# Kernel tuning notes

Measured on AMD Instinct MI355X. Metric: run time of the kernel, lower is better.

Reference implementation:

```python
import jax, jax.numpy as jnp
import numpy as np

SLEN, BSZ = 256, 8
NUM_HEAD, DIM_HEAD = 16, 64
IN_DIM = NUM_HEAD * DIM_HEAD  # 1024
LN_EPS = 1e-5


def setup_inputs() -> dict:
    key = jax.random.key(0)
    ks = jax.random.split(key, 6)
    std = 1.0 / np.sqrt(DIM_HEAD)
    std_q = 0.01 / np.sqrt(DIM_HEAD)
    beta_init = -1.0
    h = jax.random.normal(ks[0], (SLEN, BSZ, IN_DIM), dtype=jnp.float32)
    W_y = std * jax.random.normal(ks[1], (1, NUM_HEAD, DIM_HEAD, DIM_HEAD), dtype=jnp.float32)
    W_q = std_q * jax.random.normal(ks[2], (1, NUM_HEAD, DIM_HEAD, DIM_HEAD), dtype=jnp.float32)
    W_k = std * jax.random.normal(ks[3], (1, NUM_HEAD, DIM_HEAD, DIM_HEAD), dtype=jnp.float32)
    w_b = beta_init + std * jax.random.normal(ks[4], (1, NUM_HEAD, DIM_HEAD, 4), dtype=jnp.float32)
    out_w = std * jax.random.normal(ks[5], (IN_DIM, NUM_HEAD * DIM_HEAD), dtype=jnp.float32)
    ln_gamma = jnp.ones((IN_DIM,), dtype=jnp.float32)
    ln_beta = jnp.zeros((IN_DIM,), dtype=jnp.float32)
    return {"h": h, "W_y": W_y, "W_q": W_q, "W_k": W_k, "w_b": w_b,
            "out_w": out_w, "ln_gamma": ln_gamma, "ln_beta": ln_beta}


def _srwm_scan(x, W_y, W_q, W_k, w_b):
    # x: (slen, B, H, d); fast weights broadcast over batch
    bsz = x.shape[1]
    Wy0 = jnp.broadcast_to(W_y, (bsz,) + W_y.shape[1:])
    Wq0 = jnp.broadcast_to(W_q, (bsz,) + W_q.shape[1:])
    Wk0 = jnp.broadcast_to(W_k, (bsz,) + W_k.shape[1:])
    wb0 = jnp.broadcast_to(w_b, (bsz,) + w_b.shape[1:])

    def step(carry, x_t):
        Wy, Wq, Wk, wb = carry
        # generate outputs with W_{t-1}
        y = jnp.einsum('bhij,bhj->bhi', Wy, x_t)
        q = jax.nn.softmax(jnp.einsum('bhij,bhj->bhi', Wq, x_t), axis=-1)
        k = jax.nn.softmax(jnp.einsum('bhij,bhj->bhi', Wk, x_t), axis=-1)
        beta = jax.nn.sigmoid(jnp.einsum('bhjc,bhj->bhc', wb, x_t))  # (B,H,4)
        qmk = q - k
        def upd(W, b):
            dv = jnp.einsum('bhij,bhj->bhi', W, qmk)  # W q - W k
            return W + b[..., None, None] * dv[..., :, None] * k[..., None, :]
        Wy_n = upd(Wy, beta[..., 0])
        Wq_n = upd(Wq, beta[..., 1])
        Wk_n = upd(Wk, beta[..., 2])
        dvb = jnp.einsum('bhjc,bhj->bhc', wb, qmk)  # (B,H,4)
        wb_n = wb + beta[..., 3][..., None, None] * k[..., :, None] * dvb[..., None, :]
        return (Wy_n, Wq_n, Wk_n, wb_n), y

    _, ys = jax.lax.scan(step, (Wy0, Wq0, Wk0, wb0), x)
    return ys  # (slen, B, H, d)


def reference(h, W_y, W_q, W_k, w_b, out_w, ln_gamma, ln_beta):
    slen, bsz, _ = h.shape
    x = h.reshape(slen, bsz, NUM_HEAD, DIM_HEAD)
    ys = _srwm_scan(x, W_y, W_q, W_k, w_b)
    out = ys.reshape(slen, bsz, NUM_HEAD * DIM_HEAD)
    out = out @ out_w.T  # (slen, bsz, in_dim), no bias
    # dropout p=0 (eval): identity
    mu = jnp.mean(h, axis=-1, keepdims=True)
    var = jnp.mean(jnp.square(h - mu), axis=-1, keepdims=True)
    h_ln = (h - mu) * jax.lax.rsqrt(var + LN_EPS) * ln_gamma + ln_beta
    return h_ln + out
```

## Files before the change

### kernel.cpp

```cpp
#include <hip/hip_runtime.h>
#include <hip/hip_bf16.h>

#define SLEN  256
#define BSZ   8
#define NHEAD 16
#define DHEAD 64
#define INDIM 1024
#define LN_EPS 1e-5f

typedef __attribute__((ext_vector_type(4))) float f32x4;
typedef __attribute__((ext_vector_type(8))) short bf16x8;
typedef __attribute__((ext_vector_type(2))) float v2f;

__device__ __forceinline__ int f_as_i(float f) { union { float f; int i; } u; u.f = f; return u.i; }
__device__ __forceinline__ float i_as_f(int i) { union { float f; int i; } u; u.i = i; return u.f; }

__device__ __forceinline__ v2f fma2(v2f a, v2f b, v2f c) {
  return __builtin_elementwise_fma(a, b, c);
}

__device__ inline unsigned short f2bf(float x) {
  __hip_bfloat16 b = __float2bfloat16(x);
  union { __hip_bfloat16 b; unsigned short u; } cv;
  cv.b = b;
  return cv.u;
}

template <int CTRL>
__device__ __forceinline__ float dpp0(float x) {
  return i_as_f(__builtin_amdgcn_update_dpp(0, f_as_i(x), CTRL, 0xF, 0xF, true));
}
__device__ __forceinline__ float pair_other(float x) { return dpp0<0xB1>(x); }

__device__ __forceinline__ float wave_sum64(float v) {
  v += dpp0<0x111>(v);
  v += dpp0<0x112>(v);
  v += dpp0<0x114>(v);
  v += dpp0<0x118>(v);
  v += dpp0<0x142>(v);
  v += dpp0<0x143>(v);
  return i_as_f(__builtin_amdgcn_readlane(f_as_i(v), 63));
}

__global__ __launch_bounds__(512, 1) void scan_prep_k(
    const float* __restrict__ h,
    const float* __restrict__ Wy0,
    const float* __restrict__ Wq0,
    const float* __restrict__ Wk0,
    const float* __restrict__ wb0,
    const float* __restrict__ outw,
    const float* __restrict__ gamma,
    const float* __restrict__ lbeta,
    unsigned short* __restrict__ outw_bf,
    float* __restrict__ outp,
    unsigned short* __restrict__ ys_bf) {
  const int bid = blockIdx.x;
  const int tid = threadIdx.x;

  if (bid >= 128) {
    const int pb = bid - 128;
    if (pb < 512) {
      int i = (pb * 512 + tid) * 4;
      float4 v = *(const float4*)(outw + i);
      ushort4 o;
      o.x = f2bf(v.x); o.y = f2bf(v.y); o.z = f2bf(v.z); o.w = f2bf(v.w);
      *(ushort4*)(outw_bf + i) = o;
    } else {
      int r = pb - 512;
      const float* row = h + (size_t)r * INDIM;
      float2 v = *(const float2*)(row + tid * 2);
      float s  = v.x + v.y;
      float s2 = v.x * v.x + v.y * v.y;
      s  = wave_sum64(s);
      s2 = wave_sum64(s2);
      __shared__ float ls[8], ls2[8], sstat[2];
      int wvv = tid >> 6;
      if ((tid & 63) == 0) { ls[wvv] = s; ls2[wvv] = s2; }
      __syncthreads();
      if (tid == 0) {
        float S = 0.f, S2 = 0.f;
        #pragma unroll
        for (int i2 = 0; i2 < 8; ++i2) { S += ls[i2]; S2 += ls2[i2]; }
        float mu = S * (1.0f / INDIM);
        float var = S2 * (1.0f / INDIM) - mu * mu;
        sstat[0] = mu;
        sstat[1] = rsqrtf(var + LN_EPS);
      }
      __syncthreads();
      float mu = sstat[0], rs = sstat[1];
      float2 g2 = *(const float2*)(gamma + tid * 2);
      float2 b2 = *(const float2*)(lbeta + tid * 2);
      float2 o;
      o.x = (v.x - mu) * rs * g2.x + b2.x;
      o.y = (v.y - mu) * rs * g2.y + b2.y;
      *(float2*)(outp + (size_t)r * INDIM + tid * 2) = o;
    }
    return;
  }

  const int chain = bid;
  const int b    = chain >> 4;
  const int head = chain & 15;
  const int wv   = __builtin_amdgcn_readfirstlane(tid >> 6);
  const int lane = tid & 63;

  __shared__ __align__(16) float xbuf[3][64];
  __shared__ __align__(16) float eqk[2][2][64];
  __shared__ __align__(16) float meta[2][8];

  const float* xrow0 = h + (size_t)b * INDIM + head * DHEAD;

#define PUBLISH(T, V) {                                                          \
    if (m == 0) {                                                                \
      if (!(lane & 1))                                                           \
        ys_bf[(size_t)((T) * BSZ + b) * INDIM + head * DHEAD + r] = f2bf(V);     \
    } else {                                                                     \
      float e_ = __expf(V);                                                      \
      if (!(lane & 1)) eqk[(T) & 1][m - 1][r] = e_;                              \
      float sh_ = wave_sum64(e_) * 0.5f;                                         \
      if (lane == 0) meta[(T) & 1][(m - 1) * 2 + half] = sh_;                    \
    }                                                                            \
  }

#define PHASE(T, XC, XN) {                                                       \
    const int bp_ = ((T) - 1) & 1;                                               \
    float4 ss4 = *(const float4*)(&meta[bp_][0]);                                \
    float4 bb4 = *(const float4*)(&meta[bp_][4]);                                \
    v2f q2[16], k2[16];                                                          \
    _Pragma("unroll")                                                            \
    for (int g = 0; g < 8; ++g) {                                                \
      float4 qq = *(const float4*)(&eqk[bp_][0][j0 + g * 4]);                    \
      float4 kk = *(const float4*)(&eqk[bp_][1][j0 + g * 4]);                    \
      q2[2 * g] = (v2f){qq.x, qq.y}; q2[2 * g + 1] = (v2f){qq.z, qq.w};          \
      k2[2 * g] = (v2f){kk.x, kk.y}; k2[2 * g + 1] = (v2f){kk.z, kk.w};          \
    }                                                                            \
    if ((T) + 1 < SLEN) {                                                        \
      const float* xsrc_ = &xbuf[((T) + 1) % 3][j0];                             \
      _Pragma("unroll")                                                          \
      for (int g = 0; g < 8; ++g) {                                              \
        float4 x4_ = *(const float4*)(xsrc_ + g * 4);                            \
        XN[2 * g] = (v2f){x4_.x, x4_.y}; XN[2 * g + 1] = (v2f){x4_.z, x4_.w};    \
      }                                                                          \
    }                                                                            \
    v2f dqa = (v2f){0.f, 0.f}, dqb = (v2f){0.f, 0.f};                            \
    v2f dka = (v2f){0.f, 0.f}, dkb = (v2f){0.f, 0.f};                            \
    _Pragma("unroll")                                                            \
    for (int g = 0; g < 16; g += 2) {                                            \
      dqa = fma2(w2[g], q2[g], dqa);                                             \
      dqb = fma2(w2[g + 1], q2[g + 1], dqb);                                     \
      dka = fma2(w2[g], k2[g], dka);                                             \
      dkb = fma2(w2[g + 1], k2[g + 1], dkb);                                     \
    }                                                                            \
    float rq = __fdividef(1.f, ss4.x + ss4.y);                                   \
    float rk = __fdividef(1.f, ss4.z + ss4.w);                                   \
    v2f dqs = dqa + dqb, dks = dka + dkb;                                        \
    float dv = rq * (dqs.x + dqs.y) - rk * (dks.x + dks.y);                      \
    dv += pair_other(dv);                                                        \
    float bet_ = (m == 0) ? bb4.x : ((m == 1) ? bb4.y : bb4.z);                  \
    float c_ = bet_ * dv * rk;                                                   \
    v2f c2 = (v2f){c_, c_};                                                      \
    _Pragma("unroll")                                                            \
    for (int g = 0; g < 16; ++g) w2[g] = fma2(c2, k2[g], w2[g]);                 \
    v2f aa = (v2f){0.f, 0.f}, ab = (v2f){0.f, 0.f};                              \
    _Pragma("unroll")                                                            \
    for (int g = 0; g < 16; g += 2) {                                            \
      aa = fma2(w2[g], XC[g], aa);                                               \
      ab = fma2(w2[g + 1], XC[g + 1], ab);                                       \
    }                                                                            \
    v2f as = aa + ab;                                                            \
    float v_ = as.x + as.y;                                                      \
    v_ += pair_other(v_);                                                        \
    PUBLISH(T, v_);                                                              \
    __syncthreads();                                                             \
  }

  if (wv < 6) {
    const int m    = wv >> 1;
    const int half = wv & 1;
    const int r    = half * 32 + (lane >> 1);
    const int j0   = (lane & 1) * 32;
    const float* Wsel = (m == 0) ? Wy0 : ((m == 1) ? Wq0 : Wk0);
    const float* wrow = Wsel + (size_t)head * DHEAD * DHEAD + (size_t)r * DHEAD + j0;
    v2f w2[16];
    #pragma unroll
    for (int g = 0; g < 8; ++g) {
      float4 t4 = *(const float4*)(wrow + g * 4);
      w2[2 * g] = (v2f){t4.x, t4.y}; w2[2 * g + 1] = (v2f){t4.z, t4.w};
    }
    v2f xA[16], xB[16];
    #pragma unroll
    for (int g = 0; g < 8; ++g) {
      float4 t4 = *(const float4*)(xrow0 + j0 + g * 4);
      xA[2 * g] = (v2f){t4.x, t4.y}; xA[2 * g + 1] = (v2f){t4.z, t4.w};
    }
    __syncthreads();

    {
      v2f aa = (v2f){0.f, 0.f}, ab = (v2f){0.f, 0.f};
      #pragma unroll
      for (int g = 0; g < 16; g += 2) {
        aa = fma2(w2[g], xA[g], aa);
        ab = fma2(w2[g + 1], xA[g + 1], ab);
      }
      v2f as = aa + ab;
      float v0 = as.x + as.y;
      v0 += pair_other(v0);
      PUBLISH(0, v0);
      #pragma unroll
      for (int g = 0; g < 8; ++g) {
        float4 x4 = *(const float4*)(&xbuf[1][j0 + g * 4]);
        xB[2 * g] = (v2f){x4.x, x4.y}; xB[2 * g + 1] = (v2f){x4.z, x4.w};
      }
      __syncthreads();
    }
    for (int tt = 1; tt <= 253; tt += 2) {
      PHASE(tt, xB, xA);
      PHASE(tt + 1, xA, xB);
    }
    PHASE(255, xB, xA);
  } else if (wv == 6) {
    const float* wbrow = wb0 + (size_t)head * DHEAD * 4 + lane * 4;
    float4 wbv = *(const float4*)wbrow;
    const float* xl = h + (size_t)b * INDIM + head * DHEAD + lane;
    float xv = xl[0];
    float xn = xl[(size_t)BSZ * INDIM];
    float b3prev = 0.f;
    __syncthreads();

    {
      float p0 = wave_sum64(wbv.x * xv);
      float p1 = wave_sum64(wbv.y * xv);
      float p2 = wave_sum64(wbv.z * xv);
      float p3 = wave_sum64(wbv.w * xv);
      float b0 = __fdividef(1.f, 1.f + __expf(-p0));
      float b1 = __fdividef(1.f, 1.f + __expf(-p1));
      float b2 = __fdividef(1.f, 1.f + __expf(-p2));
      float b3 = __fdividef(1.f, 1.f + __expf(-p3));
      if (lane == 0) *(float4*)(&meta[0][4]) = (float4){b0, b1, b2, b3};
      b3prev = b3;
      xv = xn;
      xn = xl[(size_t)2 * BSZ * INDIM];
      __syncthreads();
    }
    for (int t = 1; t < SLEN; ++t) {
      const int bp = (t - 1) & 1;
      float4 ss4 = *(const float4*)(&meta[bp][0]);
      float eq = eqk[bp][0][lane];
      float ek = eqk[bp][1][lane];
      float rq = __fdividef(1.f, ss4.x + ss4.y);
      float rk = __fdividef(1.f, ss4.z + ss4.w);
      float qv = rq * eq, kv = rk * ek;
      float qmk = qv - kv;
      float g0 = wave_sum64(wbv.x * qmk);
      float g1 = wave_sum64(wbv.y * qmk);
      float g2 = wave_sum64(wbv.z * qmk);
      float g3 = wave_sum64(wbv.w * qmk);
      float cl = b3prev * kv;
      wbv.x += cl * g0; wbv.y += cl * g1; wbv.z += cl * g2; wbv.w += cl * g3;
      float p0 = wave_sum64(wbv.x * xv);
      float p1 = wave_sum64(wbv.y * xv);
      float p2 = wave_sum64(wbv.z * xv);
      float p3 = wave_sum64(wbv.w * xv);
      float b0 = __fdividef(1.f, 1.f + __expf(-p0));
      float b1 = __fdividef(1.f, 1.f + __expf(-p1));
      float b2 = __fdividef(1.f, 1.f + __expf(-p2));
      float b3 = __fdividef(1.f, 1.f + __expf(-p3));
      if (lane == 0) *(float4*)(&meta[t & 1][4]) = (float4){b0, b1, b2, b3};
      b3prev = b3;
      xv = xn;
      if (t + 2 < SLEN) xn = xl[(size_t)(t + 2) * BSZ * INDIM];
      __syncthreads();
    }
  } else {
    xbuf[1][lane] = xrow0[(size_t)BSZ * INDIM + lane];
    xbuf[2][lane] = xrow0[(size_t)2 * BSZ * INDIM + lane];
    float g1 = xrow0[(size_t)3 * BSZ * INDIM + lane];
    __syncthreads();

    for (int t = 0; t < SLEN; ++t) {
      if (t + 3 < SLEN) xbuf[t % 3][lane] = g1;
      if (t + 4 < SLEN) g1 = xrow0[(size_t)(t + 4) * BSZ * INDIM + lane];
      __syncthreads();
    }
  }
#undef PHASE
#undef PUBLISH
}

#define LDA 40
__global__ __launch_bounds__(256, 2) void gemm_acc_k(
    const unsigned short* __restrict__ A,
    const unsigned short* __restrict__ B,
    float* __restrict__ out,
    float scale) {
  __shared__ __align__(16) unsigned short Al[2][64 * LDA];
  __shared__ __align__(16) unsigned short Bl[2][64 * LDA];

  const int bid0 = blockIdx.x;
  const int swz = (bid0 & 7) * 64 + (bid0 >> 3);
  const int bx = swz & 15;
  const int by = swz >> 4;
  const int tid = threadIdx.x;
  const int wave = tid >> 6, lane = tid & 63;
  const int wr = wave >> 1, wc = wave & 1;
  const int l16 = lane & 15;
  const int kofs = (lane >> 4) * 8;

  const short* Ap = (const short*)A;
  const short* Bp = (const short*)B;

  const int srow = tid >> 2;
  const int scol = (tid & 3) * 8;
  const short* ags = Ap + (size_t)(by * 64 + srow) * INDIM + scol;
  const short* bgs = Bp + (size_t)(bx * 64 + srow) * INDIM + scol;
  unsigned short* adst = &Al[0][srow * LDA + scol];
  unsigned short* bdst = &Bl[0][srow * LDA + scol];

  f32x4 acc[2][2];
  #pragma unroll
  for (int i = 0; i < 2; ++i)
    #pragma unroll
    for (int j = 0; j < 2; ++j)
      acc[i][j] = (f32x4){0.f, 0.f, 0.f, 0.f};

  {
    uint4 ga = *(const uint4*)(ags);
    uint4 gb = *(const uint4*)(bgs);
    *(uint4*)(adst) = ga;
    *(uint4*)(bdst) = gb;
  }
  __syncthreads();

  int buf = 0;
  for (int it = 0; it < 32; ++it) {
    uint4 ga, gb;
    const bool more = (it + 1 < 32);
    if (more) {
      ga = *(const uint4*)(ags + (it + 1) * 32);
      gb = *(const uint4*)(bgs + (it + 1) * 32);
    }
    bf16x8 af[2], bfv[2];
    #pragma unroll
    for (int i = 0; i < 2; ++i)
      af[i] = *(const bf16x8*)(&Al[buf][(wr * 32 + i * 16 + l16) * LDA + kofs]);
    #pragma unroll
    for (int j = 0; j < 2; ++j)
      bfv[j] = *(const bf16x8*)(&Bl[buf][(wc * 32 + j * 16 + l16) * LDA + kofs]);
    #pragma unroll
    for (int i = 0; i < 2; ++i)
      #pragma unroll
      for (int j = 0; j < 2; ++j)
        acc[i][j] = __builtin_amdgcn_mfma_f32_16x16x32_bf16(af[i], bfv[j], acc[i][j], 0, 0, 0);
    if (more) {
      *(uint4*)(adst + (buf ^ 1) * 64 * LDA) = ga;
      *(uint4*)(bdst + (buf ^ 1) * 64 * LDA) = gb;
    }
    __syncthreads();
    buf ^= 1;
  }

  const int rq4 = (lane >> 4) * 4;
  #pragma unroll
  for (int i = 0; i < 2; ++i) {
    #pragma unroll
    for (int reg = 0; reg < 4; ++reg) {
      int r = by * 64 + wr * 32 + i * 16 + rq4 + reg;
      #pragma unroll
      for (int j = 0; j < 2; ++j) {
        int n = bx * 64 + wc * 32 + j * 16 + l16;
        size_t idx = (size_t)r * INDIM + n;
        out[idx] += acc[i][j][reg] * scale;
      }
    }
  }
}

extern "C" void kernel_launch(void* const* d_in, const int* in_sizes, int n_in,
                              void* d_out, int out_size, void* d_ws, size_t ws_size,
                              hipStream_t stream) {
  const float* h    = (const float*)d_in[0];
  const float* Wy   = (const float*)d_in[1];
  const float* Wq   = (const float*)d_in[2];
  const float* Wk   = (const float*)d_in[3];
  const float* wb   = (const float*)d_in[4];
  const float* outw = (const float*)d_in[5];
  const float* gam  = (const float*)d_in[6];
  const float* bet  = (const float*)d_in[7];
  float* out = (float*)d_out;

  char* ws = (char*)d_ws;
  unsigned short* ys_bf   = (unsigned short*)ws;
  unsigned short* outw_bf = (unsigned short*)(ws + (size_t)2048 * 1024 * 2);

  scan_prep_k<<<128 + 512 + 2048, 512, 0, stream>>>(h, Wy, Wq, Wk, wb, outw,
                                                    gam, bet, outw_bf, out, ys_bf);
  gemm_acc_k<<<512, 256, 0, stream>>>(ys_bf, outw_bf, out, 1e-38f);
  gemm_acc_k<<<512, 256, 0, stream>>>(ys_bf, outw_bf, out, 1.0f);
}
```

Measured before the change: 306.9 us.

## Shorten scan step dependency chain, widen GEMM K-tile, drop duplicate GEMM launch

The scan step now computes W·x and k·x from the old weights and forms y as A + c·(k·x). This takes the post-update matvec off the serial dependency chain after the weight update, and it switches to 4-wide vector FMAs. The GEMM now uses a 64-wide K tile per stage, giving half as many barrier iterations. The extra GEMM launch with a tiny scale factor is removed, so the GEMM runs once instead of twice. The algebraic rewrite changes floating-point rounding slightly, and the larger tile uses more LDS.

```diff
diff --git a/kernel.cpp b/kernel.cpp
--- a/kernel.cpp
+++ b/kernel.cpp
@@ -10,14 +10,14 @@
 
 typedef __attribute__((ext_vector_type(4))) float f32x4;
 typedef __attribute__((ext_vector_type(8))) short bf16x8;
-typedef __attribute__((ext_vector_type(2))) float v2f;
 
 __device__ __forceinline__ int f_as_i(float f) { union { float f; int i; } u; u.f = f; return u.i; }
 __device__ __forceinline__ float i_as_f(int i) { union { float f; int i; } u; u.i = i; return u.f; }
 
-__device__ __forceinline__ v2f fma2(v2f a, v2f b, v2f c) {
+__device__ __forceinline__ f32x4 fma4(f32x4 a, f32x4 b, f32x4 c) {
   return __builtin_elementwise_fma(a, b, c);
 }
+__device__ __forceinline__ float hsum4(f32x4 a) { return (a.x + a.y) + (a.z + a.w); }
 
 __device__ inline unsigned short f2bf(float x) {
   __hip_bfloat16 b = __float2bfloat16(x);
@@ -124,52 +124,46 @@
 
 #define PHASE(T, XC, XN) {                                                       \
     const int bp_ = ((T) - 1) & 1;                                               \
+    const f32x4* eq4_ = (const f32x4*)(&eqk[bp_][0][j0]);                        \
+    const f32x4* ek4_ = (const f32x4*)(&eqk[bp_][1][j0]);                        \
+    f32x4 q4[8], k4[8];                                                          \
+    _Pragma("unroll")                                                            \
+    for (int g = 0; g < 8; ++g) { q4[g] = eq4_[g]; k4[g] = ek4_[g]; }            \
     float4 ss4 = *(const float4*)(&meta[bp_][0]);                                \
     float4 bb4 = *(const float4*)(&meta[bp_][4]);                                \
-    v2f q2[16], k2[16];                                                          \
+    if ((T) + 1 < SLEN) {                                                        \
+      const f32x4* xs_ = (const f32x4*)(&xbuf[((T) + 1) % 3][j0]);               \
+      _Pragma("unroll")                                                          \
+      for (int g = 0; g < 8; ++g) XN[g] = xs_[g];                                \
+    }                                                                            \
+    f32x4 mva = (f32x4){0.f, 0.f, 0.f, 0.f};                                     \
+    f32x4 mvb = (f32x4){0.f, 0.f, 0.f, 0.f};                                     \
+    _Pragma("unroll")                                                            \
+    for (int g = 0; g < 8; g += 2) {                                             \
+      mva = fma4(w4[g], XC[g], mva);                                             \
+      mvb = fma4(w4[g + 1], XC[g + 1], mvb);                                     \
+    }                                                                            \
+    f32x4 dqa = (f32x4){0.f, 0.f, 0.f, 0.f};                                     \
+    f32x4 dka = (f32x4){0.f, 0.f, 0.f, 0.f};                                     \
+    f32x4 exa = (f32x4){0.f, 0.f, 0.f, 0.f};                                     \
     _Pragma("unroll")                                                            \
     for (int g = 0; g < 8; ++g) {                                                \
-      float4 qq = *(const float4*)(&eqk[bp_][0][j0 + g * 4]);                    \
-      float4 kk = *(const float4*)(&eqk[bp_][1][j0 + g * 4]);                    \
-      q2[2 * g] = (v2f){qq.x, qq.y}; q2[2 * g + 1] = (v2f){qq.z, qq.w};          \
-      k2[2 * g] = (v2f){kk.x, kk.y}; k2[2 * g + 1] = (v2f){kk.z, kk.w};          \
-    }                                                                            \
-    if ((T) + 1 < SLEN) {                                                        \
-      const float* xsrc_ = &xbuf[((T) + 1) % 3][j0];                             \
-      _Pragma("unroll")                                                          \
-      for (int g = 0; g < 8; ++g) {                                              \
-        float4 x4_ = *(const float4*)(xsrc_ + g * 4);                            \
-        XN[2 * g] = (v2f){x4_.x, x4_.y}; XN[2 * g + 1] = (v2f){x4_.z, x4_.w};    \
-      }                                                                          \
-    }                                                                            \
-    v2f dqa = (v2f){0.f, 0.f}, dqb = (v2f){0.f, 0.f};                            \
-    v2f dka = (v2f){0.f, 0.f}, dkb = (v2f){0.f, 0.f};                            \
-    _Pragma("unroll")                                                            \
-    for (int g = 0; g < 16; g += 2) {                                            \
-      dqa = fma2(w2[g], q2[g], dqa);                                             \
-      dqb = fma2(w2[g + 1], q2[g + 1], dqb);                                     \
-      dka = fma2(w2[g], k2[g], dka);                                             \
-      dkb = fma2(w2[g + 1], k2[g + 1], dkb);                                     \
+      dqa = fma4(w4[g], q4[g], dqa);                                             \
+      dka = fma4(w4[g], k4[g], dka);                                             \
+      exa = fma4(k4[g], XC[g], exa);                                             \
     }                                                                            \
     float rq = __fdividef(1.f, ss4.x + ss4.y);                                   \
     float rk = __fdividef(1.f, ss4.z + ss4.w);                                   \
-    v2f dqs = dqa + dqb, dks = dka + dkb;                                        \
-    float dv = rq * (dqs.x + dqs.y) - rk * (dks.x + dks.y);                      \
+    float dv = rq * hsum4(dqa) - rk * hsum4(dka);                                \
     dv += pair_other(dv);                                                        \
     float bet_ = (m == 0) ? bb4.x : ((m == 1) ? bb4.y : bb4.z);                  \
     float c_ = bet_ * dv * rk;                                                   \
-    v2f c2 = (v2f){c_, c_};                                                      \
+    f32x4 c4_ = (f32x4){c_, c_, c_, c_};                                         \
     _Pragma("unroll")                                                            \
-    for (int g = 0; g < 16; ++g) w2[g] = fma2(c2, k2[g], w2[g]);                 \
-    v2f aa = (v2f){0.f, 0.f}, ab = (v2f){0.f, 0.f};                              \
-    _Pragma("unroll")                                                            \
-    for (int g = 0; g < 16; g += 2) {                                            \
-      aa = fma2(w2[g], XC[g], aa);                                               \
-      ab = fma2(w2[g + 1], XC[g + 1], ab);                                       \
-    }                                                                            \
-    v2f as = aa + ab;                                                            \
-    float v_ = as.x + as.y;                                                      \
-    v_ += pair_other(v_);                                                        \
+    for (int g = 0; g < 8; ++g) w4[g] = fma4(c4_, k4[g], w4[g]);                 \
+    float A_ = hsum4(mva + mvb); A_ += pair_other(A_);                           \
+    float B_ = hsum4(exa);       B_ += pair_other(B_);                           \
+    float v_ = A_ + c_ * B_;                                                     \
     PUBLISH(T, v_);                                                              \
     __syncthreads();                                                             \
   }
@@ -181,36 +175,28 @@
     const int j0   = (lane & 1) * 32;
     const float* Wsel = (m == 0) ? Wy0 : ((m == 1) ? Wq0 : Wk0);
     const float* wrow = Wsel + (size_t)head * DHEAD * DHEAD + (size_t)r * DHEAD + j0;
-    v2f w2[16];
-    #pragma unroll
-    for (int g = 0; g < 8; ++g) {
-      float4 t4 = *(const float4*)(wrow + g * 4);
-      w2[2 * g] = (v2f){t4.x, t4.y}; w2[2 * g + 1] = (v2f){t4.z, t4.w};
-    }
-    v2f xA[16], xB[16];
-    #pragma unroll
-    for (int g = 0; g < 8; ++g) {
-      float4 t4 = *(const float4*)(xrow0 + j0 + g * 4);
-      xA[2 * g] = (v2f){t4.x, t4.y}; xA[2 * g + 1] = (v2f){t4.z, t4.w};
-    }
+    f32x4 w4[8];
+    #pragma unroll
+    for (int g = 0; g < 8; ++g) w4[g] = *(const f32x4*)(wrow + g * 4);
+    f32x4 xA[8], xB[8];
+    #pragma unroll
+    for (int g = 0; g < 8; ++g) xA[g] = *(const f32x4*)(xrow0 + j0 + g * 4);
     __syncthreads();
 
     {
-      v2f aa = (v2f){0.f, 0.f}, ab = (v2f){0.f, 0.f};
-      #pragma unroll
-      for (int g = 0; g < 16; g += 2) {
-        aa = fma2(w2[g], xA[g], aa);
-        ab = fma2(w2[g + 1], xA[g + 1], ab);
+      const f32x4* xs = (const f32x4*)(&xbuf[1][j0]);
+      #pragma unroll
+      for (int g = 0; g < 8; ++g) xB[g] = xs[g];
+      f32x4 aa = (f32x4){0.f, 0.f, 0.f, 0.f};
+      f32x4 ab = (f32x4){0.f, 0.f, 0.f, 0.f};
+      #pragma unroll
+      for (int g = 0; g < 8; g += 2) {
+        aa = fma4(w4[g], xA[g], aa);
+        ab = fma4(w4[g + 1], xA[g + 1], ab);
       }
-      v2f as = aa + ab;
-      float v0 = as.x + as.y;
+      float v0 = hsum4(aa + ab);
       v0 += pair_other(v0);
       PUBLISH(0, v0);
-      #pragma unroll
-      for (int g = 0; g < 8; ++g) {
-        float4 x4 = *(const float4*)(&xbuf[1][j0 + g * 4]);
-        xB[2 * g] = (v2f){x4.x, x4.y}; xB[2 * g + 1] = (v2f){x4.z, x4.w};
-      }
       __syncthreads();
     }
     for (int tt = 1; tt <= 253; tt += 2) {
@@ -287,14 +273,13 @@
 #undef PUBLISH
 }
 
-#define LDA 40
+#define GLDA 72
 __global__ __launch_bounds__(256, 2) void gemm_acc_k(
     const unsigned short* __restrict__ A,
     const unsigned short* __restrict__ B,
-    float* __restrict__ out,
-    float scale) {
-  __shared__ __align__(16) unsigned short Al[2][64 * LDA];
-  __shared__ __align__(16) unsigned short Bl[2][64 * LDA];
+    float* __restrict__ out) {
+  __shared__ __align__(16) unsigned short Al[2][64 * GLDA];
+  __shared__ __align__(16) unsigned short Bl[2][64 * GLDA];
 
   const int bid0 = blockIdx.x;
   const int swz = (bid0 & 7) * 64 + (bid0 >> 3);
@@ -310,11 +295,11 @@
   const short* Bp = (const short*)B;
 
   const int srow = tid >> 2;
-  const int scol = (tid & 3) * 8;
+  const int scol = (tid & 3) * 16;
   const short* ags = Ap + (size_t)(by * 64 + srow) * INDIM + scol;
   const short* bgs = Bp + (size_t)(bx * 64 + srow) * INDIM + scol;
-  unsigned short* adst = &Al[0][srow * LDA + scol];
-  unsigned short* bdst = &Bl[0][srow * LDA + scol];
+  unsigned short* adst = &Al[0][srow * GLDA + scol];
+  unsigned short* bdst = &Bl[0][srow * GLDA + scol];
 
   f32x4 acc[2][2];
   #pragma unroll
@@ -324,36 +309,50 @@
       acc[i][j] = (f32x4){0.f, 0.f, 0.f, 0.f};
 
   {
-    uint4 ga = *(const uint4*)(ags);
-    uint4 gb = *(const uint4*)(bgs);
-    *(uint4*)(adst) = ga;
-    *(uint4*)(bdst) = gb;
+    uint4 a0 = *(const uint4*)(ags);
+    uint4 a1 = *(const uint4*)(ags + 8);
+    uint4 b0 = *(const uint4*)(bgs);
+    uint4 b1 = *(const uint4*)(bgs + 8);
+    *(uint4*)(adst) = a0;
+    *(uint4*)(adst + 8) = a1;
+    *(uint4*)(bdst) = b0;
+    *(uint4*)(bdst + 8) = b1;
   }
   __syncthreads();
 
   int buf = 0;
-  for (int it = 0; it < 32; ++it) {
-    uint4 ga, gb;
-    const bool more = (it + 1 < 32);
+  for (int it = 0; it < 16; ++it) {
+    uint4 a0, a1, b0, b1;
+    const bool more = (it + 1 < 16);
     if (more) {
-      ga = *(const uint4*)(ags + (it + 1) * 32);
-      gb = *(const uint4*)(bgs + (it + 1) * 32);
-    }
-    bf16x8 af[2], bfv[2];
-    #pragma unroll
-    for (int i = 0; i < 2; ++i)
-      af[i] = *(const bf16x8*)(&Al[buf][(wr * 32 + i * 16 + l16) * LDA + kofs]);
-    #pragma unroll
-    for (int j = 0; j < 2; ++j)
-      bfv[j] = *(const bf16x8*)(&Bl[buf][(wc * 32 + j * 16 + l16) * LDA + kofs]);
-    #pragma unroll
-    for (int i = 0; i < 2; ++i)
+      const int ko = (it + 1) * 64;
+      a0 = *(const uint4*)(ags + ko);
+      a1 = *(const uint4*)(ags + ko + 8);
+      b0 = *(const uint4*)(bgs + ko);
+      b1 = *(const uint4*)(bgs + ko + 8);
+    }
+    #pragma unroll
+    for (int ks = 0; ks < 2; ++ks) {
+      bf16x8 af[2], bfv[2];
+      #pragma unroll
+      for (int i = 0; i < 2; ++i)
+        af[i] = *(const bf16x8*)(&Al[buf][(wr * 32 + i * 16 + l16) * GLDA + ks * 32 + kofs]);
       #pragma unroll
       for (int j = 0; j < 2; ++j)
-        acc[i][j] = __builtin_amdgcn_mfma_f32_16x16x32_bf16(af[i], bfv[j], acc[i][j], 0, 0, 0);
+        bfv[j] = *(const bf16x8*)(&Bl[buf][(wc * 32 + j * 16 + l16) * GLDA + ks * 32 + kofs]);
+      #pragma unroll
+      for (int i = 0; i < 2; ++i)
+        #pragma unroll
+        for (int j = 0; j < 2; ++j)
+          acc[i][j] = __builtin_amdgcn_mfma_f32_16x16x32_bf16(af[i], bfv[j], acc[i][j], 0, 0, 0);
+    }
     if (more) {
-      *(uint4*)(adst + (buf ^ 1) * 64 * LDA) = ga;
-      *(uint4*)(bdst + (buf ^ 1) * 64 * LDA) = gb;
+      unsigned short* ad = adst + (buf ^ 1) * 64 * GLDA;
+      unsigned short* bd = bdst + (buf ^ 1) * 64 * GLDA;
+      *(uint4*)(ad) = a0;
+      *(uint4*)(ad + 8) = a1;
+      *(uint4*)(bd) = b0;
+      *(uint4*)(bd + 8) = b1;
     }
     __syncthreads();
     buf ^= 1;
@@ -369,7 +368,7 @@
       for (int j = 0; j < 2; ++j) {
         int n = bx * 64 + wc * 32 + j * 16 + l16;
         size_t idx = (size_t)r * INDIM + n;
-        out[idx] += acc[i][j][reg] * scale;
+        out[idx] += acc[i][j][reg];
       }
     }
   }
@@ -394,6 +393,5 @@
 
   scan_prep_k<<<128 + 512 + 2048, 512, 0, stream>>>(h, Wy, Wq, Wk, wb, outw,
                                                     gam, bet, outw_bf, out, ys_bf);
-  gemm_acc_k<<<512, 256, 0, stream>>>(ys_bf, outw_bf, out, 1e-38f);
-  gemm_acc_k<<<512, 256, 0, stream>>>(ys_bf, outw_bf, out, 1.0f);
-}
+  gemm_acc_k<<<512, 256, 0, stream>>>(ys_bf, outw_bf, out);
+}
```

New measurement: 293.1 us. 1.05x faster.
